# Kernel optimization log

Measured on AMD Instinct MI355X. Metric: run time of the kernel, lower is better.

## Reference

```python
import jax, jax.numpy as jnp
import numpy as np

N_NODES = 200000
N_EDGES = 400000
NUM_GRAPHS = 8192
NODE_DIM, EDGE_DIM, H, NCLS, NLAYERS = 80, 6, 128, 500, 4


def setup_inputs() -> dict:
    key = jax.random.key(0)
    ks = iter(jax.random.split(key, 32))
    s = 0.05
    inp = {
        "x": jax.random.normal(next(ks), (N_NODES, NODE_DIM), jnp.float32),
        "edge_index": jax.random.randint(next(ks), (2, N_EDGES), 0, N_NODES, jnp.int32),
        "edge_attr": jax.random.uniform(next(ks), (N_EDGES, EDGE_DIM), jnp.float32),
        # sorted segment ids covering all NUM_GRAPHS graphs (~24 nodes each)
        "batch": ((jnp.arange(N_NODES, dtype=jnp.int64) * NUM_GRAPHS) // N_NODES).astype(jnp.int32),
        "node_w": jax.random.normal(next(ks), (NODE_DIM, H), jnp.float32) * s,
        "node_b": jnp.zeros((H,), jnp.float32),
        "edge_w": jax.random.normal(next(ks), (EDGE_DIM, H), jnp.float32) * s,
        "edge_b": jnp.zeros((H,), jnp.float32),
        "conv_w1": jax.random.normal(next(ks), (NLAYERS, H, 2 * H), jnp.float32) * s,
        "conv_b1": jnp.zeros((NLAYERS, 2 * H), jnp.float32),
        "conv_bn1_g": jnp.ones((NLAYERS, 2 * H), jnp.float32),
        "conv_bn1_b": jnp.zeros((NLAYERS, 2 * H), jnp.float32),
        "conv_w2": jax.random.normal(next(ks), (NLAYERS, 2 * H, H), jnp.float32) * s,
        "conv_b2": jnp.zeros((NLAYERS, H), jnp.float32),
        "bn_g": jnp.ones((NLAYERS, H), jnp.float32),
        "bn_b": jnp.zeros((NLAYERS, H), jnp.float32),
        "cls_w1": jax.random.normal(next(ks), (2 * H, H), jnp.float32) * s,
        "cls_b1": jnp.zeros((H,), jnp.float32),
        "cls_bn_g": jnp.ones((H,), jnp.float32),
        "cls_bn_b": jnp.zeros((H,), jnp.float32),
        "cls_w2": jax.random.normal(next(ks), (H, NCLS), jnp.float32) * s,
        "cls_b2": jnp.zeros((NCLS,), jnp.float32),
    }
    return inp


def _bn(h, g, b, eps=1e-5):
    # training-mode BatchNorm1d: biased batch statistics over dim 0
    m = h.mean(0)
    v = h.var(0)
    return (h - m) * jax.lax.rsqrt(v + eps) * g + b


def reference(x, edge_index, edge_attr, batch,
              node_w, node_b, edge_w, edge_b,
              conv_w1, conv_b1, conv_bn1_g, conv_bn1_b,
              conv_w2, conv_b2, bn_g, bn_b,
              cls_w1, cls_b1, cls_bn_g, cls_bn_b, cls_w2, cls_b2):
    n = x.shape[0]
    h = x @ node_w + node_b                       # [N, H]
    ea = edge_attr @ edge_w + edge_b              # [E, H]
    src, dst = edge_index[0], edge_index[1]       # PyG: row=source j, col=target i
    for l in range(conv_w1.shape[0]):
        # GINEConv: nn((1+eps)*x + sum_j relu(x_j + e_ij)), eps=0
        msg = jax.nn.relu(h[src] + ea)            # [E, H] gather + add + relu
        agg = jax.ops.segment_sum(msg, dst, num_segments=n)
        z = h + agg
        z = jax.nn.relu(_bn(z @ conv_w1[l] + conv_b1[l], conv_bn1_g[l], conv_bn1_b[l]))
        h = z @ conv_w2[l] + conv_b2[l]
        h = jax.nn.relu(_bn(h, bn_g[l], bn_b[l]))
    # global mean + max pooling over graphs
    counts = jax.ops.segment_sum(jnp.ones((n, 1), h.dtype), batch, num_segments=NUM_GRAPHS)
    pmean = jax.ops.segment_sum(h, batch, num_segments=NUM_GRAPHS) / jnp.maximum(counts, 1.0)
    pmax = jax.ops.segment_max(h, batch, num_segments=NUM_GRAPHS)
    pmax = jnp.where(jnp.isfinite(pmax), pmax, 0.0)
    p = jnp.concatenate([pmean, pmax], axis=1)    # [G, 2H]
    z = jax.nn.relu(p @ cls_w1 + cls_b1)
    z = _bn(z, cls_bn_g, cls_bn_b)                # dropout: identity (eval)
    return z @ cls_w2 + cls_b2                    # [G, NCLS]
```

## Files before the change

### kernel.cpp

```cpp
#include <hip/hip_runtime.h>

#define NN 200000
#define NE 400000
#define NG 8192
#define HD 128
#define H2 256
#define ND 80
#define NC 500
#define ZBLK 240
#define NCHUNK 6250

typedef short bf16x8 __attribute__((ext_vector_type(8)));
typedef short bf16x4 __attribute__((ext_vector_type(4)));
typedef float f32x4  __attribute__((ext_vector_type(4)));

static __device__ __forceinline__ short f2bf(float f) {
    unsigned u = __float_as_uint(f);
    unsigned r = (u + 0x7fffu + ((u >> 16) & 1u)) >> 16;
    return (short)r;
}
static __device__ __forceinline__ float bf2f(short s) {
    return __uint_as_float(((unsigned)(unsigned short)s) << 16);
}

__global__ void k_zero(float* p, int n) {
    int i = blockIdx.x * 256 + threadIdx.x;
    if (i < n) p[i] = 0.f;
}

__global__ __launch_bounds__(256) void k_node_encode(
    const float* __restrict__ x, const float* __restrict__ w,
    const float* __restrict__ b, float* __restrict__ h, float* __restrict__ agg)
{
    __shared__ float ws[ND][HD];
    __shared__ float xs[32][ND];
    const int tid = threadIdx.x;
    for (int i = tid; i < ND * HD; i += 256) ws[i >> 7][i & 127] = w[i];
    const int row0 = blockIdx.x * 32;
    for (int i = tid; i < 32 * ND; i += 256) {
        int r = i / ND, c = i % ND;
        xs[r][c] = x[(size_t)(row0 + r) * ND + c];
    }
    __syncthreads();
    const int col = tid & 127, rs = tid >> 7;
    const float bias = b[col];
    for (int it = 0; it < 16; ++it) {
        int rl = it * 2 + rs;
        float acc = bias;
        #pragma unroll
        for (int k = 0; k < ND; ++k) acc += xs[rl][k] * ws[k][col];
        size_t gi = (size_t)(row0 + rl) * HD + col;
        h[gi] = acc;
        agg[gi] = 0.f;
    }
}

__global__ __launch_bounds__(256) void k_msg_agg(
    const float* __restrict__ h, const int* __restrict__ ei,
    const float* __restrict__ eattr, const float* __restrict__ ew,
    const float* __restrict__ eb, float* __restrict__ agg)
{
    __shared__ float ews[6][HD];
    __shared__ float ebs[HD];
    const int tid = threadIdx.x;
    for (int i = tid; i < 6 * HD; i += 256) ews[i >> 7][i & 127] = ew[i];
    if (tid < HD) ebs[tid] = eb[tid];
    __syncthreads();
    const int col = tid & 127, es = tid >> 7;
    const int e0 = blockIdx.x * 32;
    for (int it = 0; it < 16; ++it) {
        int e = e0 + it * 2 + es;
        int src = ei[e], dst = ei[NE + e];
        float a0 = eattr[e * 6 + 0], a1 = eattr[e * 6 + 1], a2 = eattr[e * 6 + 2];
        float a3 = eattr[e * 6 + 3], a4 = eattr[e * 6 + 4], a5 = eattr[e * 6 + 5];
        float m = h[(size_t)src * HD + col] + ebs[col]
                + a0 * ews[0][col] + a1 * ews[1][col] + a2 * ews[2][col]
                + a3 * ews[3][col] + a4 * ews[4][col] + a5 * ews[5][col];
        m = fmaxf(m, 0.f);
        atomicAdd(&agg[(size_t)dst * HD + col], m);
    }
}

__global__ __launch_bounds__(256) void k_zstats2(
    const float* __restrict__ h, const float* __restrict__ agg,
    float* __restrict__ Mpart, float* __restrict__ colzPart)
{
    __shared__ float zs[32][HD];
    __shared__ float cred[8][HD];
    const int tid = threadIdx.x;
    const int bid = blockIdx.x;
    const int i0 = (tid >> 5) * 16;
    const int j0 = (tid & 31) * 4;
    const int lrow = tid >> 5;
    const int lc4  = tid & 31;

    float acc[16][4];
    #pragma unroll
    for (int a = 0; a < 16; ++a)
        #pragma unroll
        for (int b = 0; b < 4; ++b) acc[a][b] = 0.f;
    float4 csum = make_float4(0.f, 0.f, 0.f, 0.f);

    float4 pv[4];
    int chunk = bid;
    {
        const size_t r0 = (size_t)chunk * 32;
        #pragma unroll
        for (int i = 0; i < 4; ++i) {
            size_t gi = (r0 + lrow + i * 8) * HD + lc4 * 4;
            float4 hv = *(const float4*)(h + gi);
            float4 av = *(const float4*)(agg + gi);
            pv[i] = make_float4(hv.x + av.x, hv.y + av.y, hv.z + av.z, hv.w + av.w);
        }
    }

    while (chunk < NCHUNK) {
        __syncthreads();
        #pragma unroll
        for (int i = 0; i < 4; ++i) {
            *(float4*)(&zs[lrow + i * 8][lc4 * 4]) = pv[i];
            csum.x += pv[i].x; csum.y += pv[i].y;
            csum.z += pv[i].z; csum.w += pv[i].w;
        }
        __syncthreads();
        int nxt = chunk + ZBLK;
        if (nxt < NCHUNK) {
            const size_t r0 = (size_t)nxt * 32;
            #pragma unroll
            for (int i = 0; i < 4; ++i) {
                size_t gi = (r0 + lrow + i * 8) * HD + lc4 * 4;
                float4 hv = *(const float4*)(h + gi);
                float4 av = *(const float4*)(agg + gi);
                pv[i] = make_float4(hv.x + av.x, hv.y + av.y, hv.z + av.z, hv.w + av.w);
            }
        }
        #pragma unroll 8
        for (int r = 0; r < 32; ++r) {
            float4 zj  = *(const float4*)(&zs[r][j0]);
            float4 zi0 = *(const float4*)(&zs[r][i0]);
            float4 zi1 = *(const float4*)(&zs[r][i0 + 4]);
            float4 zi2 = *(const float4*)(&zs[r][i0 + 8]);
            float4 zi3 = *(const float4*)(&zs[r][i0 + 12]);
            float zi[16] = {zi0.x, zi0.y, zi0.z, zi0.w,
                            zi1.x, zi1.y, zi1.z, zi1.w,
                            zi2.x, zi2.y, zi2.z, zi2.w,
                            zi3.x, zi3.y, zi3.z, zi3.w};
            #pragma unroll
            for (int a = 0; a < 16; ++a) {
                acc[a][0] += zi[a] * zj.x;
                acc[a][1] += zi[a] * zj.y;
                acc[a][2] += zi[a] * zj.z;
                acc[a][3] += zi[a] * zj.w;
            }
        }
        chunk = nxt;
    }

    float* mp = Mpart + (size_t)bid * 16384;
    #pragma unroll
    for (int a = 0; a < 16; ++a)
        *(float4*)(mp + (i0 + a) * HD + j0) =
            make_float4(acc[a][0], acc[a][1], acc[a][2], acc[a][3]);

    *(float4*)(&cred[lrow][lc4 * 4]) = csum;
    __syncthreads();
    if (tid < HD) {
        float s = 0.f;
        #pragma unroll
        for (int k = 0; k < 8; ++k) s += cred[k][tid];
        colzPart[bid * HD + tid] = s;
    }
}

__global__ __launch_bounds__(256) void k_mreduce(
    const float* __restrict__ Mpart, const float* __restrict__ colzPart,
    float* __restrict__ M, float* __restrict__ colz)
{
    int idx = blockIdx.x * 256 + threadIdx.x;
    if (idx < 16384) {
        float s = 0.f;
        for (int b = 0; b < ZBLK; ++b) s += Mpart[(size_t)b * 16384 + idx];
        M[idx] = s;
    } else if (idx < 16384 + HD) {
        int c = idx - 16384;
        float s = 0.f;
        for (int b = 0; b < ZBLK; ++b) s += colzPart[b * HD + c];
        colz[c] = s;
    }
}

__global__ __launch_bounds__(128) void k_bnprep1(
    const float* __restrict__ M, const float* __restrict__ colz,
    const float* __restrict__ w1p,
    const float* __restrict__ g, const float* __restrict__ b,
    float* __restrict__ scale, float* __restrict__ shift)
{
    __shared__ float wcs[128];
    __shared__ float red[128];
    __shared__ float red2[128];
    const int c = blockIdx.x;
    const int j = threadIdx.x;
    float wc = w1p[j * H2 + c];
    wcs[j] = wc;
    __syncthreads();
    float inner = 0.f;
    for (int k = 0; k < 128; ++k) inner += M[j * HD + k] * wcs[k];
    red[j] = wc * inner;
    red2[j] = colz[j] * wc;
    __syncthreads();
    for (int s = 64; s > 0; s >>= 1) {
        if (j < s) { red[j] += red[j + s]; red2[j] += red2[j + s]; }
        __syncthreads();
    }
    if (j == 0) {
        const float invn = 1.f / NN;
        float q = red[0] * invn;
        float d = red2[0] * invn;
        float var = q - d * d;
        float sc = g[c] * rsqrtf(var + 1e-5f);
        scale[c] = sc;
        shift[c] = b[c] - d * sc;
    }
}

__global__ __launch_bounds__(256) void k_wprep(
    const float* __restrict__ w1, const float* __restrict__ w2,
    short* __restrict__ wh, short* __restrict__ wlo)
{
    int id = blockIdx.x * 256 + threadIdx.x;
    int layer = id >> 16, r = id & 65535;
    float v;
    if (r < 32768) {
        int ft = r >> 11, kk = (r >> 9) & 3, l = (r >> 3) & 63, j = r & 7;
        int k = kk * 32 + (l >> 4) * 8 + j, c = ft * 16 + (l & 15);
        v = w1[(size_t)layer * HD * H2 + k * H2 + c];
    } else {
        int r2 = r - 32768;
        int ft = r2 >> 12, kk = (r2 >> 9) & 7, l = (r2 >> 3) & 63, j = r2 & 7;
        int k = kk * 32 + (l >> 4) * 8 + j, c = ft * 16 + (l & 15);
        v = w2[(size_t)layer * H2 * HD + k * HD + c];
    }
    short hi = f2bf(v);
    wh[id] = hi;
    wlo[id] = f2bf(v - bf2f(hi));
}

__global__ __launch_bounds__(128) void k_fused_mfma3(
    const float* __restrict__ h, const float* agg,
    const short* __restrict__ w1h, const short* __restrict__ w1l,
    const short* __restrict__ w2h, const short* __restrict__ w2l,
    const float* __restrict__ scale1, const float* __restrict__ shift1,
    const float* __restrict__ b2p, float* u)
{
    __shared__ short ysh[32 * 256];
    __shared__ short ysl[32 * 256];
    __shared__ float sc1s[H2], sh1s[H2];
    const int tid = threadIdx.x;
    const int row0g = blockIdx.x * 32;
    for (int i = tid; i < H2; i += 128) { sc1s[i] = scale1[i]; sh1s[i] = shift1[i]; }

    const int l = tid & 63, w = tid >> 6;
    const int nq = l >> 4;
    const int node = w * 16 + (l & 15);
    const int nx = node & 7;
    const size_t zbase = (size_t)(row0g + node) * HD;

    bf16x8 zh[4], zl[4];
    #pragma unroll
    for (int kk = 0; kk < 4; ++kk) {
        int c0 = kk * 32 + nq * 8;
        float4 h0 = *(const float4*)(h + zbase + c0);
        float4 h1 = *(const float4*)(h + zbase + c0 + 4);
        float4 a0 = *(const float4*)(agg + zbase + c0);
        float4 a1 = *(const float4*)(agg + zbase + c0 + 4);
        float z[8] = {h0.x + a0.x, h0.y + a0.y, h0.z + a0.z, h0.w + a0.w,
                      h1.x + a1.x, h1.y + a1.y, h1.z + a1.z, h1.w + a1.w};
        #pragma unroll
        for (int j = 0; j < 8; ++j) {
            short hi = f2bf(z[j]);
            zh[kk][j] = hi;
            zl[kk][j] = f2bf(z[j] - bf2f(hi));
        }
    }
    __syncthreads();

    #pragma unroll
    for (int ft = 0; ft < 16; ++ft) {
        f32x4 acc = {0.f, 0.f, 0.f, 0.f};
        #pragma unroll
        for (int kk = 0; kk < 4; ++kk) {
            int wi = ((ft * 4 + kk) * 64 + l) * 8;
            bf16x8 ah = *(const bf16x8*)(w1h + wi);
            bf16x8 al = *(const bf16x8*)(w1l + wi);
            acc = __builtin_amdgcn_mfma_f32_16x16x32_bf16(ah, zh[kk], acc, 0, 0, 0);
            acc = __builtin_amdgcn_mfma_f32_16x16x32_bf16(ah, zl[kk], acc, 0, 0, 0);
            acc = __builtin_amdgcn_mfma_f32_16x16x32_bf16(al, zh[kk], acc, 0, 0, 0);
        }
        int f0 = ft * 16 + nq * 4;
        float4 scv = *(const float4*)(&sc1s[f0]);
        float4 shv = *(const float4*)(&sh1s[f0]);
        float y0 = fmaxf(acc[0] * scv.x + shv.x, 0.f);
        float y1 = fmaxf(acc[1] * scv.y + shv.y, 0.f);
        float y2 = fmaxf(acc[2] * scv.z + shv.z, 0.f);
        float y3 = fmaxf(acc[3] * scv.w + shv.w, 0.f);
        bf16x4 ph, pl;
        ph[0] = f2bf(y0); pl[0] = f2bf(y0 - bf2f(ph[0]));
        ph[1] = f2bf(y1); pl[1] = f2bf(y1 - bf2f(ph[1]));
        ph[2] = f2bf(y2); pl[2] = f2bf(y2 - bf2f(ph[2]));
        ph[3] = f2bf(y3); pl[3] = f2bf(y3 - bf2f(ph[3]));
        int off = node * 256 + (((f0 >> 3) ^ nx) * 8) + (nq & 1) * 4;
        *(bf16x4*)(&ysh[off]) = ph;
        *(bf16x4*)(&ysl[off]) = pl;
    }
    __syncthreads();

    bf16x8 ybh[8], ybl[8];
    #pragma unroll
    for (int kk = 0; kk < 8; ++kk) {
        int off = node * 256 + (((kk * 4 + nq) ^ nx) * 8);
        ybh[kk] = *(const bf16x8*)(&ysh[off]);
        ybl[kk] = *(const bf16x8*)(&ysl[off]);
    }
    #pragma unroll
    for (int ft = 0; ft < 8; ++ft) {
        f32x4 acc = {0.f, 0.f, 0.f, 0.f};
        #pragma unroll
        for (int kk = 0; kk < 8; ++kk) {
            int wi = ((ft * 8 + kk) * 64 + l) * 8;
            bf16x8 ah = *(const bf16x8*)(w2h + wi);
            bf16x8 al = *(const bf16x8*)(w2l + wi);
            acc = __builtin_amdgcn_mfma_f32_16x16x32_bf16(ah, ybh[kk], acc, 0, 0, 0);
            acc = __builtin_amdgcn_mfma_f32_16x16x32_bf16(ah, ybl[kk], acc, 0, 0, 0);
            acc = __builtin_amdgcn_mfma_f32_16x16x32_bf16(al, ybh[kk], acc, 0, 0, 0);
        }
        int f0 = ft * 16 + nq * 4;
        float4 bv = *(const float4*)(b2p + f0);
        float4 o = make_float4(acc[0] + bv.x, acc[1] + bv.y,
                               acc[2] + bv.z, acc[3] + bv.w);
        *(float4*)(&u[(size_t)(row0g + node) * HD + f0]) = o;
    }
}

__global__ __launch_bounds__(256) void k_ustats(
    const float* __restrict__ u,
    float* __restrict__ uslotS, float* __restrict__ uslotSS)
{
    __shared__ float sS[2][HD], sQ[2][HD];
    const int tid = threadIdx.x;
    const int col = tid & 127, half = tid >> 7;
    size_t r0 = (size_t)blockIdx.x * 500 + half * 250;
    float s = 0.f, ss = 0.f;
    for (int i = 0; i < 250; ++i) {
        float v = u[(r0 + i) * HD + col];
        s += v; ss += v * v;
    }
    sS[half][col] = s; sQ[half][col] = ss;
    __syncthreads();
    if (tid < HD) {
        int slot = blockIdx.x & 63;
        atomicAdd(&uslotS[slot * HD + tid],  sS[0][tid] + sS[1][tid]);
        atomicAdd(&uslotSS[slot * HD + tid], sQ[0][tid] + sQ[1][tid]);
    }
}

__global__ __launch_bounds__(128) void k_bnprep2(
    float* __restrict__ uslotS, float* __restrict__ uslotSS,
    const float* __restrict__ g, const float* __restrict__ b,
    float* __restrict__ scale, float* __restrict__ shift)
{
    const int c = threadIdx.x;
    float s = 0.f, ss = 0.f;
    for (int k = 0; k < 64; ++k) {
        s  += uslotS[k * HD + c];
        ss += uslotSS[k * HD + c];
        uslotS[k * HD + c] = 0.f;
        uslotSS[k * HD + c] = 0.f;
    }
    const float invn = 1.f / NN;
    float mean = s * invn;
    float var = ss * invn - mean * mean;
    float sc = g[c] * rsqrtf(var + 1e-5f);
    scale[c] = sc;
    shift[c] = b[c] - mean * sc;
}

__global__ __launch_bounds__(256) void k_norm(
    const float* __restrict__ scale, const float* __restrict__ shift,
    float* __restrict__ h, float* uio)
{
    int idx = blockIdx.x * 256 + threadIdx.x;
    float4 v = ((const float4*)uio)[idx];
    int c = (idx * 4) & 127;
    v.x = fmaxf(v.x * scale[c + 0] + shift[c + 0], 0.f);
    v.y = fmaxf(v.y * scale[c + 1] + shift[c + 1], 0.f);
    v.z = fmaxf(v.z * scale[c + 2] + shift[c + 2], 0.f);
    v.w = fmaxf(v.w * scale[c + 3] + shift[c + 3], 0.f);
    ((float4*)h)[idx] = v;
    ((float4*)uio)[idx] = make_float4(0.f, 0.f, 0.f, 0.f);
}

__global__ __launch_bounds__(128) void k_pool(
    const float* __restrict__ h, const int* __restrict__ batch,
    float* __restrict__ pmean, float* __restrict__ pmax)
{
    const int g = blockIdx.x;
    const int tid = threadIdx.x;
    int lo = 0, hi = NN;
    while (lo < hi) { int mid = (lo + hi) >> 1; if (batch[mid] < g) lo = mid + 1; else hi = mid; }
    const int start = lo;
    hi = NN;
    while (lo < hi) { int mid = (lo + hi) >> 1; if (batch[mid] < g + 1) lo = mid + 1; else hi = mid; }
    const int end = lo;
    float s = 0.f, m = 0.f;
    for (int i = start; i < end; ++i) {
        float v = h[(size_t)i * HD + tid];
        s += v; m = fmaxf(m, v);
    }
    float cnt = (float)(end - start);
    pmean[g * HD + tid] = s / fmaxf(cnt, 1.f);
    pmax[g * HD + tid] = m;
}

__global__ __launch_bounds__(128) void k_cls1(
    const float* __restrict__ pmean, const float* __restrict__ pmax,
    const float* __restrict__ w, const float* __restrict__ b,
    float* __restrict__ z1)
{
    __shared__ float ps[16][H2];
    const int tid = threadIdx.x;
    const int row0 = blockIdx.x * 16;
    for (int i = tid; i < 16 * H2; i += 128) {
        int r = i >> 8, k = i & 255;
        ps[r][k] = (k < HD) ? pmean[(row0 + r) * HD + k]
                            : pmax[(row0 + r) * HD + k - HD];
    }
    __syncthreads();
    const int cp = tid & 63, rg = tid >> 6;
    float a0[8], a1[8];
    #pragma unroll
    for (int r = 0; r < 8; ++r) { a0[r] = 0.f; a1[r] = 0.f; }
    for (int kk = 0; kk < 64; ++kk) {
        float w00 = w[(kk * 4 + 0) * HD + cp];
        float w01 = w[(kk * 4 + 1) * HD + cp];
        float w02 = w[(kk * 4 + 2) * HD + cp];
        float w03 = w[(kk * 4 + 3) * HD + cp];
        float w10 = w[(kk * 4 + 0) * HD + cp + 64];
        float w11 = w[(kk * 4 + 1) * HD + cp + 64];
        float w12 = w[(kk * 4 + 2) * HD + cp + 64];
        float w13 = w[(kk * 4 + 3) * HD + cp + 64];
        #pragma unroll
        for (int r = 0; r < 8; ++r) {
            float4 z4 = *(const float4*)(&ps[rg * 8 + r][kk * 4]);
            a0[r] += z4.x * w00; a0[r] += z4.y * w01;
            a0[r] += z4.z * w02; a0[r] += z4.w * w03;
            a1[r] += z4.x * w10; a1[r] += z4.y * w11;
            a1[r] += z4.z * w12; a1[r] += z4.w * w13;
        }
    }
    const float bb0 = b[cp], bb1 = b[cp + 64];
    #pragma unroll
    for (int r = 0; r < 8; ++r) {
        int row = row0 + rg * 8 + r;
        z1[row * HD + cp]      = fmaxf(a0[r] + bb0, 0.f);
        z1[row * HD + cp + 64] = fmaxf(a1[r] + bb1, 0.f);
    }
}

__global__ __launch_bounds__(256) void k_colstats(
    const float* __restrict__ a, int nrows,
    float* __restrict__ ssum, float* __restrict__ ssumsq)
{
    const int tid = threadIdx.x;
    const int col = tid & 127;
    const int rsub = tid >> 7;
    const int r0 = blockIdx.x * 500;
    float s = 0.f, ss = 0.f;
    for (int i = rsub; i < 500; i += 2) {
        int r = r0 + i;
        if (r < nrows) {
            float v = a[r * HD + col];
            s += v; ss += v * v;
        }
    }
    atomicAdd(&ssum[col], s);
    atomicAdd(&ssumsq[col], ss);
}

__global__ void k_bnprep(float* __restrict__ ssum, float* __restrict__ ssumsq,
                         const float* __restrict__ g, const float* __restrict__ b,
                         float* __restrict__ scale, float* __restrict__ shift,
                         float invn)
{
    int c = threadIdx.x;
    if (c < HD) {
        float mean = ssum[c] * invn;
        float var = ssumsq[c] * invn - mean * mean;
        float sc = g[c] * rsqrtf(var + 1e-5f);
        scale[c] = sc;
        shift[c] = b[c] - mean * sc;
    }
}

__global__ __launch_bounds__(256) void k_cls2(
    const float* __restrict__ z1, const float* __restrict__ scale,
    const float* __restrict__ shift, const float* __restrict__ w,
    const float* __restrict__ b, float* __restrict__ outp)
{
    __shared__ float zs[16][HD];
    const int tid = threadIdx.x;
    const int row0 = blockIdx.x * 16;
    for (int i = tid; i < 16 * HD; i += 256) {
        int r = i >> 7, k = i & 127;
        zs[r][k] = z1[(row0 + r) * HD + k] * scale[k] + shift[k];
    }
    __syncthreads();
    #pragma unroll
    for (int cpass = 0; cpass < 2; ++cpass) {
        int c = tid + cpass * 256;
        if (c < NC) {
            float acc[16];
            float bb = b[c];
            #pragma unroll
            for (int r = 0; r < 16; ++r) acc[r] = bb;
            for (int k = 0; k < HD; ++k) {
                float wv = w[k * NC + c];
                #pragma unroll
                for (int r = 0; r < 16; ++r) acc[r] += zs[r][k] * wv;
            }
            #pragma unroll
            for (int r = 0; r < 16; ++r) outp[(size_t)(row0 + r) * NC + c] = acc[r];
        }
    }
}

extern "C" void kernel_launch(void* const* d_in, const int* in_sizes, int n_in,
                              void* d_out, int out_size, void* d_ws, size_t ws_size,
                              hipStream_t stream)
{
    const float* x       = (const float*)d_in[0];
    const int*   ei      = (const int*)  d_in[1];
    const float* eattr   = (const float*)d_in[2];
    const int*   batch   = (const int*)  d_in[3];
    const float* node_w  = (const float*)d_in[4];
    const float* node_b  = (const float*)d_in[5];
    const float* edge_w  = (const float*)d_in[6];
    const float* edge_b  = (const float*)d_in[7];
    const float* conv_w1 = (const float*)d_in[8];
    const float* conv_b1 = (const float*)d_in[9];
    const float* bn1g    = (const float*)d_in[10];
    const float* bn1b    = (const float*)d_in[11];
    const float* conv_w2 = (const float*)d_in[12];
    const float* conv_b2 = (const float*)d_in[13];
    const float* bng     = (const float*)d_in[14];
    const float* bnb     = (const float*)d_in[15];
    const float* cw1     = (const float*)d_in[16];
    const float* cb1     = (const float*)d_in[17];
    const float* cbg     = (const float*)d_in[18];
    const float* cbb     = (const float*)d_in[19];
    const float* cw2     = (const float*)d_in[20];
    const float* cb2     = (const float*)d_in[21];
    float* out = (float*)d_out;
    float* ws  = (float*)d_ws;

    float* h   = ws;
    float* agg = h + (size_t)NN * HD;
    float* z1  = agg + (size_t)NN * HD;
    float* st  = z1 + (size_t)NG * HD;
    float* u   = agg;

    float* uslotS  = st;
    float* uslotSS = st + 8192;
    float* clsS    = st + 16384;
    float* clsSS   = st + 16512;
    float* scale1  = st + 16640;
    float* shift1  = st + 16896;
    float* scale2  = st + 17152;
    float* shift2  = st + 17280;
    float* scalec  = st + 17408;
    float* shiftc  = st + 17536;
    float* M       = st + 17664;
    float* colz    = st + 34048;
    short* wbfh    = (short*)(st + 34176);
    short* wbfl    = (short*)(st + 34176 + 131072);

    float* Mpart    = out;
    float* colzPart = out + (size_t)ZBLK * 16384;
    float* pmean = out;
    float* pmax  = out + (size_t)NG * HD;

    k_zero<<<(16640 + 255) / 256, 256, 0, stream>>>(st, 16640);

    k_wprep<<<1024, 256, 0, stream>>>(conv_w1, conv_w2, wbfh, wbfl);

    k_node_encode<<<NN / 32, 256, 0, stream>>>(x, node_w, node_b, h, agg);

    for (int l = 0; l < 4; ++l) {
        k_msg_agg<<<NE / 32, 256, 0, stream>>>(h, ei, eattr, edge_w, edge_b, agg);
        k_zstats2<<<ZBLK, 256, 0, stream>>>(h, agg, Mpart, colzPart);
        k_mreduce<<<(16384 + HD + 255) / 256, 256, 0, stream>>>(Mpart, colzPart, M, colz);
        k_bnprep1<<<H2, 128, 0, stream>>>(M, colz,
                                          conv_w1 + (size_t)l * HD * H2,
                                          bn1g + (size_t)l * H2, bn1b + (size_t)l * H2,
                                          scale1, shift1);
        k_fused_mfma3<<<NN / 32, 128, 0, stream>>>(h, agg,
                                                   wbfh + (size_t)l * 65536,
                                                   wbfl + (size_t)l * 65536,
                                                   wbfh + (size_t)l * 65536 + 32768,
                                                   wbfl + (size_t)l * 65536 + 32768,
                                                   scale1, shift1,
                                                   conv_b2 + (size_t)l * HD, u);
        k_ustats<<<400, 256, 0, stream>>>(u, uslotS, uslotSS);
        k_bnprep2<<<1, 128, 0, stream>>>(uslotS, uslotSS,
                                         bng + (size_t)l * HD, bnb + (size_t)l * HD,
                                         scale2, shift2);
        k_norm<<<(NN * HD / 4) / 256, 256, 0, stream>>>(scale2, shift2, h, u);
    }

    k_pool<<<NG, 128, 0, stream>>>(h, batch, pmean, pmax);
    k_cls1<<<NG / 16, 128, 0, stream>>>(pmean, pmax, cw1, cb1, z1);
    k_colstats<<<17, 256, 0, stream>>>(z1, NG, clsS, clsSS);
    k_bnprep<<<1, 256, 0, stream>>>(clsS, clsSS, cbg, cbb, scalec, shiftc, 1.f / NG);
    k_cls2<<<NG / 16, 256, 0, stream>>>(z1, scalec, shiftc, cw2, cb2, out);
}
```

Baseline: 2.699 ms.

## Fold BN2+ReLU into consumers, drop normalize kernel, prefetch MFMA weights

Removes the separate k_norm pass by storing raw pre-BN output u and applying the second BatchNorm scale/shift plus ReLU lazily in the message, stats, fused MLP and pooling kernels. The fused kernel now writes u in place and zeroes agg itself, which saves a full read/write sweep of the node features per layer. It also double-buffers the weight fragment loads for both MFMA GEMMs, removes a syncthreads, and sets a minimum-occupancy launch bound. In exchange the BN affine is recomputed on every gather in message passing, and the in-place u update means each block must finish reading its own rows before it overwrites them.

```diff
diff --git a/kernel.cpp b/kernel.cpp
--- a/kernel.cpp
+++ b/kernel.cpp
@@ -30,7 +30,7 @@
 
 __global__ __launch_bounds__(256) void k_node_encode(
     const float* __restrict__ x, const float* __restrict__ w,
-    const float* __restrict__ b, float* __restrict__ h, float* __restrict__ agg)
+    const float* __restrict__ b, float* __restrict__ u, float* __restrict__ agg)
 {
     __shared__ float ws[ND][HD];
     __shared__ float xs[32][ND];
@@ -50,21 +50,22 @@
         #pragma unroll
         for (int k = 0; k < ND; ++k) acc += xs[rl][k] * ws[k][col];
         size_t gi = (size_t)(row0 + rl) * HD + col;
-        h[gi] = acc;
+        u[gi] = acc;
         agg[gi] = 0.f;
     }
 }
 
 __global__ __launch_bounds__(256) void k_msg_agg(
-    const float* __restrict__ h, const int* __restrict__ ei,
+    const float* __restrict__ u, const int* __restrict__ ei,
     const float* __restrict__ eattr, const float* __restrict__ ew,
-    const float* __restrict__ eb, float* __restrict__ agg)
+    const float* __restrict__ eb, const float* __restrict__ s2,
+    const float* __restrict__ sh2, float* __restrict__ agg, int first)
 {
     __shared__ float ews[6][HD];
-    __shared__ float ebs[HD];
+    __shared__ float ebs[HD], s2s[HD], sh2s[HD];
     const int tid = threadIdx.x;
     for (int i = tid; i < 6 * HD; i += 256) ews[i >> 7][i & 127] = ew[i];
-    if (tid < HD) ebs[tid] = eb[tid];
+    if (tid < HD) { ebs[tid] = eb[tid]; s2s[tid] = s2[tid]; sh2s[tid] = sh2[tid]; }
     __syncthreads();
     const int col = tid & 127, es = tid >> 7;
     const int e0 = blockIdx.x * 32;
@@ -73,7 +74,9 @@
         int src = ei[e], dst = ei[NE + e];
         float a0 = eattr[e * 6 + 0], a1 = eattr[e * 6 + 1], a2 = eattr[e * 6 + 2];
         float a3 = eattr[e * 6 + 3], a4 = eattr[e * 6 + 4], a5 = eattr[e * 6 + 5];
-        float m = h[(size_t)src * HD + col] + ebs[col]
+        float hv = u[(size_t)src * HD + col];
+        if (!first) hv = fmaxf(hv * s2s[col] + sh2s[col], 0.f);
+        float m = hv + ebs[col]
                 + a0 * ews[0][col] + a1 * ews[1][col] + a2 * ews[2][col]
                 + a3 * ews[3][col] + a4 * ews[4][col] + a5 * ews[5][col];
         m = fmaxf(m, 0.f);
@@ -82,8 +85,9 @@
 }
 
 __global__ __launch_bounds__(256) void k_zstats2(
-    const float* __restrict__ h, const float* __restrict__ agg,
-    float* __restrict__ Mpart, float* __restrict__ colzPart)
+    const float* __restrict__ u, const float* __restrict__ agg,
+    const float* __restrict__ s2, const float* __restrict__ sh2,
+    float* __restrict__ Mpart, float* __restrict__ colzPart, int first)
 {
     __shared__ float zs[32][HD];
     __shared__ float cred[8][HD];
@@ -94,6 +98,9 @@
     const int lrow = tid >> 5;
     const int lc4  = tid & 31;
 
+    float4 sv = *(const float4*)(s2 + lc4 * 4);
+    float4 shv = *(const float4*)(sh2 + lc4 * 4);
+
     float acc[16][4];
     #pragma unroll
     for (int a = 0; a < 16; ++a)
@@ -108,8 +115,14 @@
         #pragma unroll
         for (int i = 0; i < 4; ++i) {
             size_t gi = (r0 + lrow + i * 8) * HD + lc4 * 4;
-            float4 hv = *(const float4*)(h + gi);
+            float4 hv = *(const float4*)(u + gi);
             float4 av = *(const float4*)(agg + gi);
+            if (!first) {
+                hv.x = fmaxf(hv.x * sv.x + shv.x, 0.f);
+                hv.y = fmaxf(hv.y * sv.y + shv.y, 0.f);
+                hv.z = fmaxf(hv.z * sv.z + shv.z, 0.f);
+                hv.w = fmaxf(hv.w * sv.w + shv.w, 0.f);
+            }
             pv[i] = make_float4(hv.x + av.x, hv.y + av.y, hv.z + av.z, hv.w + av.w);
         }
     }
@@ -129,8 +142,14 @@
             #pragma unroll
             for (int i = 0; i < 4; ++i) {
                 size_t gi = (r0 + lrow + i * 8) * HD + lc4 * 4;
-                float4 hv = *(const float4*)(h + gi);
+                float4 hv = *(const float4*)(u + gi);
                 float4 av = *(const float4*)(agg + gi);
+                if (!first) {
+                    hv.x = fmaxf(hv.x * sv.x + shv.x, 0.f);
+                    hv.y = fmaxf(hv.y * sv.y + shv.y, 0.f);
+                    hv.z = fmaxf(hv.z * sv.z + shv.z, 0.f);
+                    hv.w = fmaxf(hv.w * sv.w + shv.w, 0.f);
+                }
                 pv[i] = make_float4(hv.x + av.x, hv.y + av.y, hv.z + av.z, hv.w + av.w);
             }
         }
@@ -245,12 +264,13 @@
     wlo[id] = f2bf(v - bf2f(hi));
 }
 
-__global__ __launch_bounds__(128) void k_fused_mfma3(
-    const float* __restrict__ h, const float* agg,
+__global__ __launch_bounds__(128, 2) void k_fused_mfma3(
+    const float* uin, float* agg,
     const short* __restrict__ w1h, const short* __restrict__ w1l,
     const short* __restrict__ w2h, const short* __restrict__ w2l,
     const float* __restrict__ scale1, const float* __restrict__ shift1,
-    const float* __restrict__ b2p, float* u)
+    const float* __restrict__ s2, const float* __restrict__ sh2,
+    const float* __restrict__ b2p, float* uout, int first)
 {
     __shared__ short ysh[32 * 256];
     __shared__ short ysl[32 * 256];
@@ -269,12 +289,24 @@
     #pragma unroll
     for (int kk = 0; kk < 4; ++kk) {
         int c0 = kk * 32 + nq * 8;
-        float4 h0 = *(const float4*)(h + zbase + c0);
-        float4 h1 = *(const float4*)(h + zbase + c0 + 4);
+        float4 u0 = *(const float4*)(uin + zbase + c0);
+        float4 u1 = *(const float4*)(uin + zbase + c0 + 4);
         float4 a0 = *(const float4*)(agg + zbase + c0);
         float4 a1 = *(const float4*)(agg + zbase + c0 + 4);
-        float z[8] = {h0.x + a0.x, h0.y + a0.y, h0.z + a0.z, h0.w + a0.w,
-                      h1.x + a1.x, h1.y + a1.y, h1.z + a1.z, h1.w + a1.w};
+        float z[8];
+        if (first) {
+            z[0]=u0.x+a0.x; z[1]=u0.y+a0.y; z[2]=u0.z+a0.z; z[3]=u0.w+a0.w;
+            z[4]=u1.x+a1.x; z[5]=u1.y+a1.y; z[6]=u1.z+a1.z; z[7]=u1.w+a1.w;
+        } else {
+            float4 s0 = *(const float4*)(s2 + c0);
+            float4 s1 = *(const float4*)(s2 + c0 + 4);
+            float4 t0 = *(const float4*)(sh2 + c0);
+            float4 t1 = *(const float4*)(sh2 + c0 + 4);
+            z[0]=fmaxf(u0.x*s0.x+t0.x,0.f)+a0.x; z[1]=fmaxf(u0.y*s0.y+t0.y,0.f)+a0.y;
+            z[2]=fmaxf(u0.z*s0.z+t0.z,0.f)+a0.z; z[3]=fmaxf(u0.w*s0.w+t0.w,0.f)+a0.w;
+            z[4]=fmaxf(u1.x*s1.x+t1.x,0.f)+a1.x; z[5]=fmaxf(u1.y*s1.y+t1.y,0.f)+a1.y;
+            z[6]=fmaxf(u1.z*s1.z+t1.z,0.f)+a1.z; z[7]=fmaxf(u1.w*s1.w+t1.w,0.f)+a1.w;
+        }
         #pragma unroll
         for (int j = 0; j < 8; ++j) {
             short hi = f2bf(z[j]);
@@ -284,17 +316,30 @@
     }
     __syncthreads();
 
+    bf16x8 pah[2][4], pal[2][4];
+    #pragma unroll
+    for (int kk = 0; kk < 4; ++kk) {
+        int wi = (kk * 64 + l) * 8;
+        pah[0][kk] = *(const bf16x8*)(w1h + wi);
+        pal[0][kk] = *(const bf16x8*)(w1l + wi);
+    }
     #pragma unroll
     for (int ft = 0; ft < 16; ++ft) {
+        const int cur = ft & 1, nxt = cur ^ 1;
+        if (ft < 15) {
+            #pragma unroll
+            for (int kk = 0; kk < 4; ++kk) {
+                int wi = (((ft + 1) * 4 + kk) * 64 + l) * 8;
+                pah[nxt][kk] = *(const bf16x8*)(w1h + wi);
+                pal[nxt][kk] = *(const bf16x8*)(w1l + wi);
+            }
+        }
         f32x4 acc = {0.f, 0.f, 0.f, 0.f};
         #pragma unroll
         for (int kk = 0; kk < 4; ++kk) {
-            int wi = ((ft * 4 + kk) * 64 + l) * 8;
-            bf16x8 ah = *(const bf16x8*)(w1h + wi);
-            bf16x8 al = *(const bf16x8*)(w1l + wi);
-            acc = __builtin_amdgcn_mfma_f32_16x16x32_bf16(ah, zh[kk], acc, 0, 0, 0);
-            acc = __builtin_amdgcn_mfma_f32_16x16x32_bf16(ah, zl[kk], acc, 0, 0, 0);
-            acc = __builtin_amdgcn_mfma_f32_16x16x32_bf16(al, zh[kk], acc, 0, 0, 0);
+            acc = __builtin_amdgcn_mfma_f32_16x16x32_bf16(pah[cur][kk], zh[kk], acc, 0, 0, 0);
+            acc = __builtin_amdgcn_mfma_f32_16x16x32_bf16(pah[cur][kk], zl[kk], acc, 0, 0, 0);
+            acc = __builtin_amdgcn_mfma_f32_16x16x32_bf16(pal[cur][kk], zh[kk], acc, 0, 0, 0);
         }
         int f0 = ft * 16 + nq * 4;
         float4 scv = *(const float4*)(&sc1s[f0]);
@@ -312,7 +357,6 @@
         *(bf16x4*)(&ysh[off]) = ph;
         *(bf16x4*)(&ysl[off]) = pl;
     }
-    __syncthreads();
 
     bf16x8 ybh[8], ybl[8];
     #pragma unroll
@@ -321,23 +365,41 @@
         ybh[kk] = *(const bf16x8*)(&ysh[off]);
         ybl[kk] = *(const bf16x8*)(&ysl[off]);
     }
-    #pragma unroll
-    for (int ft = 0; ft < 8; ++ft) {
-        f32x4 acc = {0.f, 0.f, 0.f, 0.f};
-        #pragma unroll
-        for (int kk = 0; kk < 8; ++kk) {
-            int wi = ((ft * 8 + kk) * 64 + l) * 8;
-            bf16x8 ah = *(const bf16x8*)(w2h + wi);
-            bf16x8 al = *(const bf16x8*)(w2l + wi);
-            acc = __builtin_amdgcn_mfma_f32_16x16x32_bf16(ah, ybh[kk], acc, 0, 0, 0);
-            acc = __builtin_amdgcn_mfma_f32_16x16x32_bf16(ah, ybl[kk], acc, 0, 0, 0);
-            acc = __builtin_amdgcn_mfma_f32_16x16x32_bf16(al, ybh[kk], acc, 0, 0, 0);
-        }
-        int f0 = ft * 16 + nq * 4;
-        float4 bv = *(const float4*)(b2p + f0);
-        float4 o = make_float4(acc[0] + bv.x, acc[1] + bv.y,
-                               acc[2] + bv.z, acc[3] + bv.w);
-        *(float4*)(&u[(size_t)(row0g + node) * HD + f0]) = o;
+    bf16x8 qh[2][4], ql[2][4];
+    #pragma unroll
+    for (int kk = 0; kk < 4; ++kk) {
+        int wi = (kk * 64 + l) * 8;
+        qh[0][kk] = *(const bf16x8*)(w2h + wi);
+        ql[0][kk] = *(const bf16x8*)(w2l + wi);
+    }
+    f32x4 acc = {0.f, 0.f, 0.f, 0.f};
+    #pragma unroll
+    for (int ch = 0; ch < 16; ++ch) {
+        const int ft = ch >> 1, half = ch & 1, cur = ch & 1, nxt = cur ^ 1;
+        if (ch < 15) {
+            int ft2 = (ch + 1) >> 1, kb = ((ch + 1) & 1) * 4;
+            #pragma unroll
+            for (int kk = 0; kk < 4; ++kk) {
+                int wi = ((ft2 * 8 + kb + kk) * 64 + l) * 8;
+                qh[nxt][kk] = *(const bf16x8*)(w2h + wi);
+                ql[nxt][kk] = *(const bf16x8*)(w2l + wi);
+            }
+        }
+        if (half == 0) { acc[0] = 0.f; acc[1] = 0.f; acc[2] = 0.f; acc[3] = 0.f; }
+        #pragma unroll
+        for (int kk = 0; kk < 4; ++kk) {
+            acc = __builtin_amdgcn_mfma_f32_16x16x32_bf16(qh[cur][kk], ybh[half*4+kk], acc, 0, 0, 0);
+            acc = __builtin_amdgcn_mfma_f32_16x16x32_bf16(qh[cur][kk], ybl[half*4+kk], acc, 0, 0, 0);
+            acc = __builtin_amdgcn_mfma_f32_16x16x32_bf16(ql[cur][kk], ybh[half*4+kk], acc, 0, 0, 0);
+        }
+        if (half == 1) {
+            int f0 = ft * 16 + nq * 4;
+            float4 bv = *(const float4*)(b2p + f0);
+            float4 o = make_float4(acc[0] + bv.x, acc[1] + bv.y,
+                                   acc[2] + bv.z, acc[3] + bv.w);
+            *(float4*)(&uout[zbase + f0]) = o;
+            *(float4*)(&agg[zbase + f0]) = make_float4(0.f, 0.f, 0.f, 0.f);
+        }
     }
 }
 
@@ -384,27 +446,14 @@
     shift[c] = b[c] - mean * sc;
 }
 
-__global__ __launch_bounds__(256) void k_norm(
-    const float* __restrict__ scale, const float* __restrict__ shift,
-    float* __restrict__ h, float* uio)
-{
-    int idx = blockIdx.x * 256 + threadIdx.x;
-    float4 v = ((const float4*)uio)[idx];
-    int c = (idx * 4) & 127;
-    v.x = fmaxf(v.x * scale[c + 0] + shift[c + 0], 0.f);
-    v.y = fmaxf(v.y * scale[c + 1] + shift[c + 1], 0.f);
-    v.z = fmaxf(v.z * scale[c + 2] + shift[c + 2], 0.f);
-    v.w = fmaxf(v.w * scale[c + 3] + shift[c + 3], 0.f);
-    ((float4*)h)[idx] = v;
-    ((float4*)uio)[idx] = make_float4(0.f, 0.f, 0.f, 0.f);
-}
-
 __global__ __launch_bounds__(128) void k_pool(
-    const float* __restrict__ h, const int* __restrict__ batch,
+    const float* __restrict__ u, const int* __restrict__ batch,
+    const float* __restrict__ s2, const float* __restrict__ sh2,
     float* __restrict__ pmean, float* __restrict__ pmax)
 {
     const int g = blockIdx.x;
     const int tid = threadIdx.x;
+    const float sc = s2[tid], sh = sh2[tid];
     int lo = 0, hi = NN;
     while (lo < hi) { int mid = (lo + hi) >> 1; if (batch[mid] < g) lo = mid + 1; else hi = mid; }
     const int start = lo;
@@ -413,7 +462,7 @@
     const int end = lo;
     float s = 0.f, m = 0.f;
     for (int i = start; i < end; ++i) {
-        float v = h[(size_t)i * HD + tid];
+        float v = fmaxf(u[(size_t)i * HD + tid] * sc + sh, 0.f);
         s += v; m = fmaxf(m, v);
     }
     float cnt = (float)(end - start);
@@ -562,11 +611,10 @@
     float* out = (float*)d_out;
     float* ws  = (float*)d_ws;
 
-    float* h   = ws;
-    float* agg = h + (size_t)NN * HD;
+    float* u   = ws;
+    float* agg = u + (size_t)NN * HD;
     float* z1  = agg + (size_t)NN * HD;
     float* st  = z1 + (size_t)NG * HD;
-    float* u   = agg;
 
     float* uslotS  = st;
     float* uslotSS = st + 8192;
@@ -589,34 +637,34 @@
     float* pmax  = out + (size_t)NG * HD;
 
     k_zero<<<(16640 + 255) / 256, 256, 0, stream>>>(st, 16640);
-
     k_wprep<<<1024, 256, 0, stream>>>(conv_w1, conv_w2, wbfh, wbfl);
-
-    k_node_encode<<<NN / 32, 256, 0, stream>>>(x, node_w, node_b, h, agg);
+    k_node_encode<<<NN / 32, 256, 0, stream>>>(x, node_w, node_b, u, agg);
 
     for (int l = 0; l < 4; ++l) {
-        k_msg_agg<<<NE / 32, 256, 0, stream>>>(h, ei, eattr, edge_w, edge_b, agg);
-        k_zstats2<<<ZBLK, 256, 0, stream>>>(h, agg, Mpart, colzPart);
+        int first = (l == 0) ? 1 : 0;
+        k_msg_agg<<<NE / 32, 256, 0, stream>>>(u, ei, eattr, edge_w, edge_b,
+                                               scale2, shift2, agg, first);
+        k_zstats2<<<ZBLK, 256, 0, stream>>>(u, agg, scale2, shift2,
+                                            Mpart, colzPart, first);
         k_mreduce<<<(16384 + HD + 255) / 256, 256, 0, stream>>>(Mpart, colzPart, M, colz);
         k_bnprep1<<<H2, 128, 0, stream>>>(M, colz,
                                           conv_w1 + (size_t)l * HD * H2,
                                           bn1g + (size_t)l * H2, bn1b + (size_t)l * H2,
                                           scale1, shift1);
-        k_fused_mfma3<<<NN / 32, 128, 0, stream>>>(h, agg,
+        k_fused_mfma3<<<NN / 32, 128, 0, stream>>>(u, agg,
                                                    wbfh + (size_t)l * 65536,
                                                    wbfl + (size_t)l * 65536,
                                                    wbfh + (size_t)l * 65536 + 32768,
                                                    wbfl + (size_t)l * 65536 + 32768,
-                                                   scale1, shift1,
-                                                   conv_b2 + (size_t)l * HD, u);
+                                                   scale1, shift1, scale2, shift2,
+                                                   conv_b2 + (size_t)l * HD, u, first);
         k_ustats<<<400, 256, 0, stream>>>(u, uslotS, uslotSS);
         k_bnprep2<<<1, 128, 0, stream>>>(uslotS, uslotSS,
                                          bng + (size_t)l * HD, bnb + (size_t)l * HD,
                                          scale2, shift2);
-        k_norm<<<(NN * HD / 4) / 256, 256, 0, stream>>>(scale2, shift2, h, u);
-    }
-
-    k_pool<<<NG, 128, 0, stream>>>(h, batch, pmean, pmax);
+    }
+
+    k_pool<<<NG, 128, 0, stream>>>(u, batch, scale2, shift2, pmean, pmax);
     k_cls1<<<NG / 16, 128, 0, stream>>>(pmean, pmax, cw1, cb1, z1);
     k_colstats<<<17, 256, 0, stream>>>(z1, NG, clsS, clsSS);
     k_bnprep<<<1, 256, 0, stream>>>(clsS, clsSS, cbg, cbb, scalec, shiftc, 1.f / NG);
```

Result: no change. 2.660 ms (-1.5%).
